# Performance work log

Measured on AMD Instinct MI355X. Metric: run time of the kernel, lower is better.

The kernel has to match this reference:

```python
import jax, jax.numpy as jnp
import numpy as np

N, IN, H, HN = 20000, 256, 128, 4
S, K, B, M = 5, 2, 1024, 16
D = H * HN
ALPHA = 0.2
K_OF_S = np.array([0, 0, 1, 1, 1])  # metapath index for each global step
SPLITS = [(0, 2), (2, 5)]           # step ranges: [0,1,0]->2 steps, [0,2,1,0]->3 steps


def lrelu(z):
    return jnp.where(z >= 0, z, ALPHA * z)


def semantic_attention(z, p1w, p1b, p2w):
    # z: [B, P, D] -> Linear(D,H) -> tanh -> Linear(H,1,no bias) -> softmax over P -> weighted sum
    w = jnp.tanh(jnp.einsum('bpd,hd->bph', z, p1w) + p1b)
    s = jnp.einsum('bph,h->bp', w, p2w)
    beta = jax.nn.softmax(s, axis=1)
    return jnp.einsum('bp,bpd->bd', beta, z)


def setup_inputs():
    key = jax.random.key(0)
    ks = jax.random.split(key, 24)
    def g(k, shape, scale=1.0):
        return jax.random.normal(k, shape, dtype=jnp.float32) * scale
    s_in, s_h, s_d = IN ** -0.5, H ** -0.5, D ** -0.5
    return {
        'x': g(ks[0], (N, IN)),
        'target_nodes_mask': jax.random.randint(ks[1], (B,), 0, N),
        'neighbors': jax.random.randint(ks[2], (S, B, M), 0, N),
        # TransformerLayer params, stacked over (global step, head)
        'fc_w': g(ks[3], (S, HN, H, IN), s_in), 'fc_b': g(ks[4], (S, HN, H), 0.01),
        'q_w': g(ks[5], (S, HN, H, H), s_h), 'q_b': g(ks[6], (S, HN, H), 0.01),
        'k_w': g(ks[7], (S, HN, H, H), s_h), 'k_b': g(ks[8], (S, HN, H), 0.01),
        'v_w': g(ks[9], (S, HN, H, H), s_h), 'v_b': g(ks[10], (S, HN, H), 0.01),
        # AttentionLayer params, stacked over (metapath, head); shared across steps of a metapath
        'att_W': g(ks[11], (K, HN, H, H), s_h),
        'att_fc1_w': g(ks[12], (K, HN, H, H), s_h), 'att_fc1_b': g(ks[13], (K, HN, H), 0.01),
        'att_fc2_w': g(ks[14], (K, HN, H, H), s_h), 'att_fc2_b': g(ks[15], (K, HN, H), 0.01),
        # SemanticAttention params
        'inner_p1_w': g(ks[16], (K, H, D), s_d), 'inner_p1_b': g(ks[17], (K, H), 0.01),
        'inner_p2_w': g(ks[18], (K, H), s_h),
        'btw_p1_w': g(ks[19], (H, D), s_d), 'btw_p1_b': g(ks[20], (H,), 0.01),
        'btw_p2_w': g(ks[21], (H,), s_h),
    }


def reference(x, target_nodes_mask, neighbors, fc_w, fc_b, q_w, q_b, k_w, k_b, v_w, v_b,
              att_W, att_fc1_w, att_fc1_b, att_fc2_w, att_fc2_b,
              inner_p1_w, inner_p1_b, inner_p2_w, btw_p1_w, btw_p1_b, btw_p2_w):
    # eval mode: dropout is identity
    tx = x[target_nodes_mask]                                                             # [B,IN]
    ny = x[neighbors]                                                                     # [S,B,M,IN]
    # shared fc per (step, head) applied to both target and neighbors, then leakyrelu
    x_sh = lrelu(jnp.einsum('bi,shoi->shbo', tx, fc_w) + fc_b[:, :, None, :])             # [S,HN,B,H]
    y_sh = lrelu(jnp.einsum('sbmi,shoi->shbmo', ny, fc_w) + fc_b[:, :, None, None, :])    # [S,HN,B,M,H]
    qh = jnp.einsum('shbd,shod->shbo', x_sh, q_w) + q_b[:, :, None, :]                    # [S,HN,B,H]
    kh = jnp.einsum('shbmd,shod->shbmo', y_sh, k_w) + k_b[:, :, None, None, :]            # [S,HN,B,M,H]
    vh = jnp.einsum('shbmd,shod->shbmo', y_sh, v_w) + v_b[:, :, None, None, :]            # [S,HN,B,M,H]
    # gather per-metapath attention params to per-step layout
    aW, a1w, a1b, a2w, a2b = (p[K_OF_S] for p in (att_W, att_fc1_w, att_fc1_b, att_fc2_w, att_fc2_b))
    # AttentionLayer(key, query): bilinear score h1 @ (W @ h2^T)
    h1 = lrelu(jnp.einsum('shbmd,shod->shbmo', kh, a1w) + a1b[:, :, None, None, :])       # [S,HN,B,M,H]
    h2 = lrelu(jnp.einsum('shbd,shod->shbo', qh, a2w) + a2b[:, :, None, :])               # [S,HN,B,H]
    wh2 = jnp.einsum('shij,shbj->shbi', aW, h2)
    att = jnp.einsum('shbmd,shbd->shbm', h1, wh2)                                         # [S,HN,B,M]
    e = jax.nn.softmax(att, axis=-1)                                                      # softmax over neighbors
    h = jnp.sum(lrelu(vh * e[..., None]), axis=3)                                         # [S,HN,B,H]
    out = (x_sh + h) * 0.5
    out = jnp.transpose(out, (0, 2, 1, 3)).reshape(S, B, D)                               # head concat -> [S,B,D]
    mp = []
    for ki, (s0, s1) in enumerate(SPLITS):
        z = jnp.transpose(out[s0:s1], (1, 0, 2))                                          # [B,P_k,D]
        mp.append(semantic_attention(z, inner_p1_w[ki], inner_p1_b[ki], inner_p2_w[ki]))
    z = jnp.stack(mp, axis=1)                                                             # [B,K,D]
    return semantic_attention(z, btw_p1_w, btw_p1_b, btw_p2_w)                            # [B,D]
```

## Files before the change

kernel.cpp:

```cpp
#include <hip/hip_runtime.h>
#include <hip/hip_bf16.h>

constexpr int IN_ = 256, H_ = 128, HN_ = 4;
constexpr int S_ = 5, B_ = 1024, M_ = 16, D_ = 512;

typedef __attribute__((ext_vector_type(8))) short bf16x8;
typedef __attribute__((ext_vector_type(4))) float f32x4;
typedef __attribute__((ext_vector_type(4))) short s16x4;

__device__ __forceinline__ float lrelu(float z) { return z >= 0.f ? z : 0.2f * z; }
__device__ __forceinline__ short f2b(float f) {
    unsigned u = __float_as_uint(f);
    u += 0x7FFF + ((u >> 16) & 1);
    return (short)(u >> 16);
}
__device__ __forceinline__ float b2f(short s) {
    return __uint_as_float(((unsigned)(unsigned short)s) << 16);
}


template<int K, int ACT, bool TLDS, bool TGLB>
__device__ __forceinline__ void gemm_ldsA(
    const short* A, const short* __restrict__ W, const float* __restrict__ bias,
    short* C_lds, short* __restrict__ C_glob, int lane)
{
    f32x4 acc[8];
#pragma unroll
    for (int i = 0; i < 8; ++i) acc[i] = (f32x4){0.f, 0.f, 0.f, 0.f};
    const int m16 = lane & 15;
    const int kg  = (lane >> 4) * 8;
    const short* Ab = A + m16 * K;
    const int aswz = (m16 & 7) << 3;
#pragma unroll
    for (int kk = 0; kk < K; kk += 32) {
        bf16x8 afr = *(const bf16x8*)(Ab + ((kk + kg) ^ aswz));
        const short* Wb = W + (size_t)m16 * K + kk + kg;
#pragma unroll
        for (int cb = 0; cb < 8; ++cb) {
            bf16x8 bf = *(const bf16x8*)(Wb + (size_t)cb * 16 * K);
            acc[cb] = __builtin_amdgcn_mfma_f32_16x16x32_bf16(afr, bf, acc[cb], 0, 0, 0);
        }
    }
    const int r0 = (lane >> 4) * 4;
#pragma unroll
    for (int cb = 0; cb < 8; ++cb) {
        const int col = cb * 16 + m16;
        const float bv = bias ? bias[col] : 0.f;
#pragma unroll
        for (int i = 0; i < 4; ++i) {
            const int r = r0 + i;
            float v = acc[cb][i] + bv;
            if (ACT) v = lrelu(v);
            const short bs = f2b(v);
            if (TLDS) C_lds[r * H_ + (col ^ ((r & 7) << 3))] = bs;
            if (TGLB) C_glob[(size_t)r * H_ + col] = bs;
        }
    }
}

template<int ACT>
__device__ __forceinline__ void tile_gemm256(
    const short* Asrc, const short* __restrict__ W, const float* __restrict__ bias,
    short* Cdst, int lane, int rbase, int colb)
{
    f32x4 acc[2][2];
#pragma unroll
    for (int a = 0; a < 2; ++a)
#pragma unroll
        for (int b = 0; b < 2; ++b) acc[a][b] = (f32x4){0.f, 0.f, 0.f, 0.f};
    const int m16 = lane & 15, kg = (lane >> 4) * 8;
#pragma unroll
    for (int kk = 0; kk < 8; ++kk) {
        const int k0 = kk * 32 + kg;
        bf16x8 af[2];
#pragma unroll
        for (int rg = 0; rg < 2; ++rg) {
            const int row = rbase + rg * 16 + m16;
            af[rg] = *(const bf16x8*)(Asrc + row * 256 + (k0 ^ ((row & 7) << 3)));
        }
#pragma unroll
        for (int cbl = 0; cbl < 2; ++cbl) {
            const int col = colb + cbl * 16 + m16;
            bf16x8 bf = *(const bf16x8*)(W + (size_t)col * 256 + k0);
#pragma unroll
            for (int rg = 0; rg < 2; ++rg)
                acc[rg][cbl] = __builtin_amdgcn_mfma_f32_16x16x32_bf16(af[rg], bf, acc[rg][cbl], 0, 0, 0);
        }
    }
#pragma unroll
    for (int cbl = 0; cbl < 2; ++cbl) {
        const int col = colb + cbl * 16 + m16;
        const float bv = bias[col];
#pragma unroll
        for (int rg = 0; rg < 2; ++rg)
#pragma unroll
            for (int i = 0; i < 4; ++i) {
                const int row = rbase + rg * 16 + (lane >> 4) * 4 + i;
                float v = acc[rg][cbl][i] + bv;
                if (ACT) v = lrelu(v);
                Cdst[row * 128 + (col ^ ((row & 7) << 3))] = f2b(v);
            }
    }
}

template<int ACT, bool MIDBAR>
__device__ __forceinline__ void tile_gemm128(
    const short* Asrc, const short* __restrict__ W, const float* __restrict__ bias,
    short* Cdst, int lane, int rbase, int colb)
{
    f32x4 acc[2][2];
#pragma unroll
    for (int a = 0; a < 2; ++a)
#pragma unroll
        for (int b = 0; b < 2; ++b) acc[a][b] = (f32x4){0.f, 0.f, 0.f, 0.f};
    const int m16 = lane & 15, kg = (lane >> 4) * 8;
#pragma unroll
    for (int kk = 0; kk < 4; ++kk) {
        const int k0 = kk * 32 + kg;
        bf16x8 af[2];
#pragma unroll
        for (int rg = 0; rg < 2; ++rg) {
            const int row = rbase + rg * 16 + m16;
            af[rg] = *(const bf16x8*)(Asrc + row * 128 + (k0 ^ ((row & 7) << 3)));
        }
#pragma unroll
        for (int cbl = 0; cbl < 2; ++cbl) {
            const int col = colb + cbl * 16 + m16;
            bf16x8 bf = *(const bf16x8*)(W + (size_t)col * 128 + k0);
#pragma unroll
            for (int rg = 0; rg < 2; ++rg)
                acc[rg][cbl] = __builtin_amdgcn_mfma_f32_16x16x32_bf16(af[rg], bf, acc[rg][cbl], 0, 0, 0);
        }
    }
    if (MIDBAR) __syncthreads();
#pragma unroll
    for (int cbl = 0; cbl < 2; ++cbl) {
        const int col = colb + cbl * 16 + m16;
        const float bv = bias[col];
#pragma unroll
        for (int rg = 0; rg < 2; ++rg)
#pragma unroll
            for (int i = 0; i < 4; ++i) {
                const int row = rbase + rg * 16 + (lane >> 4) * 4 + i;
                float v = acc[rg][cbl][i] + bv;
                if (ACT) v = lrelu(v);
                Cdst[row * 128 + (col ^ ((row & 7) << 3))] = f2b(v);
            }
    }
}

__global__ __launch_bounds__(256) void k_convert(
    const float* f0, const float* f1, const float* f2, const float* f3,
    const float* f4, const float* f5, const float* f6,
    short* g0, short* g1, short* g2, short* g3, short* g4, short* g5, short* g6)
{
    const float* s; short* d; int n;
    switch (blockIdx.y) {
        case 0: s = f0; d = g0; n = 655360; break;
        case 1: s = f1; d = g1; n = 327680; break;
        case 2: s = f2; d = g2; n = 327680; break;
        case 3: s = f3; d = g3; n = 327680; break;
        case 4: s = f4; d = g4; n = 131072; break;
        case 5: s = f5; d = g5; n = 131072; break;
        default: s = f6; d = g6; n = 131072; break;
    }
    int i = (blockIdx.x * 256 + threadIdx.x) * 4;
    if (i >= n) return;
    float4 v = *(const float4*)(s + i);
    s16x4 p; p.x = f2b(v.x); p.y = f2b(v.y); p.z = f2b(v.z); p.w = f2b(v.w);
    *(s16x4*)(d + i) = p;
}

__global__ __launch_bounds__(256) void k_transpose(
    const float* __restrict__ ip1w, const float* __restrict__ bp1w,
    float* __restrict__ ipT, float* __restrict__ bpT)
{
    int i = blockIdx.x * 256 + threadIdx.x;
    if (i < 131072) {
        const int d = i & 511, hk = i >> 9;
        const int ki = hk >> 7, h = hk & 127;
        ipT[ki * 65536 + d * 128 + h] = ip1w[i];
    } else if (i < 131072 + 65536) {
        const int j = i - 131072;
        const int d = j & 511, h = j >> 9;
        bpT[d * 128 + h] = bp1w[j];
    }
}

__global__ __launch_bounds__(256) void k_target(
    const float* __restrict__ x, const int* __restrict__ tgt,
    const short* __restrict__ wb_fc, const float* __restrict__ fc_b,
    const short* __restrict__ wb_q,  const float* __restrict__ q_b,
    const short* __restrict__ wb_a2, const float* __restrict__ a2_b,
    const short* __restrict__ wb_aW,
    short* __restrict__ x_shb, short* __restrict__ wh2b)
{
    const int t = threadIdx.x, lane = t & 63, w = t >> 6;
    const int bt = blockIdx.x, s = blockIdx.y;
    const int km = (s < 2) ? 0 : 1;
    const int b0 = bt * 16;
    const int sh = s * HN_ + w, kh = km * HN_ + w;

    __shared__ __align__(16) short A[16 * 256];
    __shared__ __align__(16) short BUF[4 * 2048];
    short* buf0 = BUF + w * 2048;

    {
        const int row = t >> 4, q4 = t & 15;
        const int g = tgt[b0 + row];
        const float* xr = x + (size_t)g * IN_ + q4 * 16;
        short* arow = A + row * 256;
        const int key = (row & 7) << 3;
#pragma unroll
        for (int j = 0; j < 4; ++j) {
            float4 u = *(const float4*)(xr + j * 4);
            const int c = q4 * 16 + j * 4;
            s16x4 p; p.x = f2b(u.x); p.y = f2b(u.y); p.z = f2b(u.z); p.w = f2b(u.w);
            *(s16x4*)(arow + (c ^ key)) = p;
        }
    }
    __syncthreads();

    gemm_ldsA<256, 1, true, true>(A, wb_fc + (size_t)sh * 32768, fc_b + sh * H_,
                                  buf0, x_shb + ((size_t)sh * B_ + b0) * H_, lane);
    gemm_ldsA<128, 0, true, false>(buf0, wb_q + (size_t)sh * 16384, q_b + sh * H_,
                                   buf0, nullptr, lane);
    gemm_ldsA<128, 1, true, false>(buf0, wb_a2 + (size_t)kh * 16384, a2_b + kh * H_,
                                   buf0, nullptr, lane);
    gemm_ldsA<128, 0, false, true>(buf0, wb_aW + (size_t)kh * 16384, nullptr,
                                   nullptr, wh2b + ((size_t)sh * B_ + b0) * H_, lane);
}

__global__ __launch_bounds__(512) void k_fused(
    const float* __restrict__ x, const int* __restrict__ nbr,
    const short* __restrict__ wb_fc, const float* __restrict__ fc_b,
    const short* __restrict__ wb_k,  const float* __restrict__ k_b,
    const short* __restrict__ wb_v,  const float* __restrict__ v_b,
    const short* __restrict__ wb_a1, const float* __restrict__ a1_b,
    const short* __restrict__ x_shb, const short* __restrict__ wh2b,
    float* __restrict__ out_sbd)
{
    const int t = threadIdx.x, lane = t & 63, w = t >> 6;
    const int bt = blockIdx.x, s = blockIdx.y;
    const int km = (s < 2) ? 0 : 1;
    const int r0 = bt * 64;
    const int b0 = bt * 4;
    const int wr = w >> 2;
    const int wc = w & 3;

    __shared__ __align__(16) short A[64 * 256];
    __shared__ __align__(16) short Yt[64 * 128];
    __shared__ __align__(16) short KH[64 * 128];
    __shared__ __align__(16) short VH[64 * 128];

    {
        const int row = t >> 3, q = t & 7;
        const int g = nbr[(size_t)s * (B_ * M_) + r0 + row];
        const float* xr = x + (size_t)g * IN_ + q * 32;
        short* arow = A + row * 256;
        const int key = (row & 7) << 3;
#pragma unroll
        for (int j = 0; j < 8; ++j) {
            float4 u = *(const float4*)(xr + j * 4);
            const int c = q * 32 + j * 4;
            s16x4 p; p.x = f2b(u.x); p.y = f2b(u.y); p.z = f2b(u.z); p.w = f2b(u.w);
            *(s16x4*)(arow + (c ^ key)) = p;
        }
    }
    __syncthreads();

    const int rbase = wr * 32, colb = wc * 32;

    for (int h = 0; h < HN_; ++h) {
        const int sh = s * HN_ + h, kh = km * HN_ + h;

        tile_gemm256<1>(A, wb_fc + (size_t)sh * 32768, fc_b + sh * H_, Yt, lane, rbase, colb);
        __syncthreads();
        tile_gemm128<0, false>(Yt, wb_k + (size_t)sh * 16384, k_b + sh * H_, KH, lane, rbase, colb);
        tile_gemm128<0, false>(Yt, wb_v + (size_t)sh * 16384, v_b + sh * H_, VH, lane, rbase, colb);
        __syncthreads();
        tile_gemm128<1, true>(KH, wb_a1 + (size_t)kh * 16384, a1_b + kh * H_, KH, lane, rbase, colb);
        __syncthreads();

        {
            const int b_loc = w & 3, dhalf = w >> 2;
            const int b = b0 + b_loc;
            const short* wrow = wh2b + ((size_t)sh * B_ + b) * H_;
            const int mloc = lane >> 2;
            const int row  = b_loc * 16 + mloc;
            const int key  = (mloc & 7) << 3;
            float sc = 0.f;
#pragma unroll
            for (int j8 = 0; j8 < 4; ++j8) {
                const int c = (lane & 3) * 32 + j8 * 8;
                bf16x8 hv = *(const bf16x8*)(KH + row * 128 + (c ^ key));
                bf16x8 wv = *(const bf16x8*)(wrow + c);
#pragma unroll
                for (int e2 = 0; e2 < 8; ++e2) sc += b2f(hv[e2]) * b2f(wv[e2]);
            }
            sc += __shfl_xor(sc, 1);
            sc += __shfl_xor(sc, 2);
            float mx = sc;
            mx = fmaxf(mx, __shfl_xor(mx, 4));
            mx = fmaxf(mx, __shfl_xor(mx, 8));
            mx = fmaxf(mx, __shfl_xor(mx, 16));
            mx = fmaxf(mx, __shfl_xor(mx, 32));
            const float es = expf(sc - mx);
            float ss = es;
            ss += __shfl_xor(ss, 4);
            ss += __shfl_xor(ss, 8);
            ss += __shfl_xor(ss, 16);
            ss += __shfl_xor(ss, 32);
            const float inv = 1.f / ss;

            const short* xrow = x_shb + ((size_t)sh * B_ + b) * H_;
            float* orow = out_sbd + ((size_t)s * B_ + b) * D_ + h * H_;
            const int d = dhalf * 64 + lane;
            float hacc = 0.f;
#pragma unroll
            for (int mm = 0; mm < 16; ++mm) {
                const float e_mm = __shfl(es, mm * 4) * inv;
                const float vv = b2f(VH[(b_loc * 16 + mm) * 128 + (d ^ ((mm & 7) << 3))]);
                hacc += lrelu(vv * e_mm);
            }
            orow[d] = (b2f(xrow[d]) + hacc) * 0.5f;
        }
        __syncthreads();
    }
}

__global__ __launch_bounds__(256) void k_semantic(
    const float* __restrict__ out_sbd,
    const float* __restrict__ ipT, const float* __restrict__ ip1b,
    const float* __restrict__ ip2w,
    const float* __restrict__ bpT, const float* __restrict__ bp1b,
    const float* __restrict__ bp2w,
    float* __restrict__ out)
{
    const int b = blockIdx.x, t = threadIdx.x;
    const int h = t & 127, dh = t >> 7;
    __shared__ float zs[S_ * D_];
    __shared__ float red[2 * 128 * 8];
    __shared__ float mps[2 * D_];
    __shared__ float svals[8];
    __shared__ float beta_s[8];

    for (int idx = t; idx < S_ * D_ / 4; idx += 256) {
        int sidx = idx >> 7, c = idx & 127;
        ((float4*)zs)[idx] = ((const float4*)(out_sbd + ((size_t)sidx * B_ + b) * D_))[c];
    }
    __syncthreads();

    {
        float a0 = 0.f, a1 = 0.f, a2 = 0.f, a3 = 0.f, a4 = 0.f;
        const float* w0 = ipT + h;
        const float* w1 = ipT + 65536 + h;
        const int dbeg = dh * 256;
        for (int d = dbeg; d < dbeg + 256; ++d) {
            const float wv0 = w0[d * 128];
            const float wv1 = w1[d * 128];
            a0 += wv0 * zs[d];
            a1 += wv0 * zs[512 + d];
            a2 += wv1 * zs[1024 + d];
            a3 += wv1 * zs[1536 + d];
            a4 += wv1 * zs[2048 + d];
        }
        float* rr = red + (dh * 128 + h) * 8;
        rr[0] = a0; rr[1] = a1; rr[2] = a2; rr[3] = a3; rr[4] = a4;
    }
    __syncthreads();
    if (t < 128) {
#pragma unroll
        for (int p = 0; p < 5; ++p) {
            const int ki = (p < 2) ? 0 : 1;
            float tot = red[t * 8 + p] + red[(128 + t) * 8 + p] + ip1b[ki * 128 + t];
            red[t * 8 + p] = tanhf(tot) * ip2w[ki * 128 + t];
        }
    }
    __syncthreads();
    if (t < 64) {
#pragma unroll
        for (int p = 0; p < 5; ++p) {
            float v = red[t * 8 + p] + red[(t + 64) * 8 + p];
            v += __shfl_xor(v, 1);  v += __shfl_xor(v, 2);  v += __shfl_xor(v, 4);
            v += __shfl_xor(v, 8);  v += __shfl_xor(v, 16); v += __shfl_xor(v, 32);
            if (t == 0) svals[p] = v;
        }
    }
    __syncthreads();
    if (t == 0) {
        float mx = fmaxf(svals[0], svals[1]);
        float e0 = expf(svals[0] - mx), e1 = expf(svals[1] - mx);
        float iv = 1.f / (e0 + e1);
        beta_s[0] = e0 * iv; beta_s[1] = e1 * iv;
        mx = fmaxf(fmaxf(svals[2], svals[3]), svals[4]);
        e0 = expf(svals[2] - mx); e1 = expf(svals[3] - mx); float e2 = expf(svals[4] - mx);
        iv = 1.f / (e0 + e1 + e2);
        beta_s[2] = e0 * iv; beta_s[3] = e1 * iv; beta_s[4] = e2 * iv;
    }
    __syncthreads();
    for (int d = t; d < D_; d += 256) {
        mps[d]       = beta_s[0] * zs[d]        + beta_s[1] * zs[512 + d];
        mps[512 + d] = beta_s[2] * zs[1024 + d] + beta_s[3] * zs[1536 + d] + beta_s[4] * zs[2048 + d];
    }
    __syncthreads();

    {
        float c0 = 0.f, c1 = 0.f;
        const float* wb = bpT + h;
        const int dbeg = dh * 256;
        for (int d = dbeg; d < dbeg + 256; ++d) {
            const float wv = wb[d * 128];
            c0 += wv * mps[d];
            c1 += wv * mps[512 + d];
        }
        float* rr = red + (dh * 128 + h) * 8;
        rr[0] = c0; rr[1] = c1;
    }
    __syncthreads();
    if (t < 128) {
#pragma unroll
        for (int p = 0; p < 2; ++p) {
            float tot = red[t * 8 + p] + red[(128 + t) * 8 + p] + bp1b[t];
            red[t * 8 + p] = tanhf(tot) * bp2w[t];
        }
    }
    __syncthreads();
    if (t < 64) {
#pragma unroll
        for (int p = 0; p < 2; ++p) {
            float v = red[t * 8 + p] + red[(t + 64) * 8 + p];
            v += __shfl_xor(v, 1);  v += __shfl_xor(v, 2);  v += __shfl_xor(v, 4);
            v += __shfl_xor(v, 8);  v += __shfl_xor(v, 16); v += __shfl_xor(v, 32);
            if (t == 0) svals[p] = v;
        }
    }
    __syncthreads();
    if (t == 0) {
        float mx = fmaxf(svals[0], svals[1]);
        float e0 = expf(svals[0] - mx), e1 = expf(svals[1] - mx);
        float iv = 1.f / (e0 + e1);
        beta_s[0] = e0 * iv; beta_s[1] = e1 * iv;
    }
    __syncthreads();
    for (int d = t; d < D_; d += 256)
        out[(size_t)b * D_ + d] = beta_s[0] * mps[d] + beta_s[1] * mps[512 + d];
}

extern "C" void kernel_launch(void* const* d_in, const int* in_sizes, int n_in,
                              void* d_out, int out_size, void* d_ws, size_t ws_size,
                              hipStream_t stream)
{
    const float* x    = (const float*)d_in[0];
    const int*   tgt  = (const int*)d_in[1];
    const int*   nbr  = (const int*)d_in[2];
    const float* fc_w = (const float*)d_in[3];
    const float* fc_b = (const float*)d_in[4];
    const float* q_w  = (const float*)d_in[5];
    const float* q_b  = (const float*)d_in[6];
    const float* k_w  = (const float*)d_in[7];
    const float* k_b  = (const float*)d_in[8];
    const float* v_w  = (const float*)d_in[9];
    const float* v_b  = (const float*)d_in[10];
    const float* attW = (const float*)d_in[11];
    const float* a1w  = (const float*)d_in[12];
    const float* a1b  = (const float*)d_in[13];
    const float* a2w  = (const float*)d_in[14];
    const float* a2b  = (const float*)d_in[15];
    const float* ip1w = (const float*)d_in[16];
    const float* ip1b = (const float*)d_in[17];
    const float* ip2w = (const float*)d_in[18];
    const float* bp1w = (const float*)d_in[19];
    const float* bp1b = (const float*)d_in[20];
    const float* bp2w = (const float*)d_in[21];

    float* out = (float*)d_out;

    short* wb_fc = (short*)d_ws;
    short* wb_q  = wb_fc + 655360;
    short* wb_k  = wb_q + 327680;
    short* wb_v  = wb_k + 327680;
    short* wb_aW = wb_v + 327680;
    short* wb_a1 = wb_aW + 131072;
    short* wb_a2 = wb_a1 + 131072;
    short* x_shb = wb_a2 + 131072;
    short* wh2b  = x_shb + 2621440;
    float* out_sbd = (float*)(wh2b + 2621440);
    float* ipT   = out_sbd + 2621440;
    float* bpT   = ipT + 131072;

    k_convert<<<dim3(640, 7), 256, 0, stream>>>(
        fc_w, q_w, k_w, v_w, attW, a1w, a2w,
        wb_fc, wb_q, wb_k, wb_v, wb_aW, wb_a1, wb_a2);
    k_transpose<<<dim3(768), 256, 0, stream>>>(ip1w, bp1w, ipT, bpT);
    k_target<<<dim3(64, 5), 256, 0, stream>>>(
        x, tgt, wb_fc, fc_b, wb_q, q_b, wb_a2, a2b, wb_aW, x_shb, wh2b);
    k_fused<<<dim3(256, 5), 512, 0, stream>>>(
        x, nbr, wb_fc, fc_b, wb_k, k_b, wb_v, v_b, wb_a1, a1b, x_shb, wh2b, out_sbd);
    k_semantic<<<dim3(B_), 256, 0, stream>>>(
        out_sbd, ipT, ip1b, ip2w, bpT, bp1b, bp2w, out);
}
```

Before: 457.5 us.

## Pre-convert x to bf16 and gather neighbor rows directly from global in fc GEMM

Adds a kernel that converts all of x to bf16 once. The fused kernel then drops its 32KB LDS staging buffer and reads the gathered neighbor rows straight from global memory inside the fc GEMM, which frees LDS for higher occupancy. The a1 output now goes to Yt instead of overwriting KH in place, so the mid-GEMM barrier can be removed. In exchange, the full 20000x256 x is converted every call (about 20MB of fp32 read) even though only gathered rows are needed, and A operands are re-read from global or L2 once per head.

```diff
diff --git a/kernel.cpp b/kernel.cpp
--- a/kernel.cpp
+++ b/kernel.cpp
@@ -59,8 +59,9 @@
 }
 
 template<int ACT>
-__device__ __forceinline__ void tile_gemm256(
-    const short* Asrc, const short* __restrict__ W, const float* __restrict__ bias,
+__device__ __forceinline__ void tile_gemm256g(
+    const short* __restrict__ xr0, const short* __restrict__ xr1,
+    const short* __restrict__ W, const float* __restrict__ bias,
     short* Cdst, int lane, int rbase, int colb)
 {
     f32x4 acc[2][2];
@@ -72,19 +73,14 @@
 #pragma unroll
     for (int kk = 0; kk < 8; ++kk) {
         const int k0 = kk * 32 + kg;
-        bf16x8 af[2];
-#pragma unroll
-        for (int rg = 0; rg < 2; ++rg) {
-            const int row = rbase + rg * 16 + m16;
-            af[rg] = *(const bf16x8*)(Asrc + row * 256 + (k0 ^ ((row & 7) << 3)));
-        }
+        bf16x8 af0 = *(const bf16x8*)(xr0 + kk * 32);
+        bf16x8 af1 = *(const bf16x8*)(xr1 + kk * 32);
 #pragma unroll
         for (int cbl = 0; cbl < 2; ++cbl) {
             const int col = colb + cbl * 16 + m16;
             bf16x8 bf = *(const bf16x8*)(W + (size_t)col * 256 + k0);
-#pragma unroll
-            for (int rg = 0; rg < 2; ++rg)
-                acc[rg][cbl] = __builtin_amdgcn_mfma_f32_16x16x32_bf16(af[rg], bf, acc[rg][cbl], 0, 0, 0);
+            acc[0][cbl] = __builtin_amdgcn_mfma_f32_16x16x32_bf16(af0, bf, acc[0][cbl], 0, 0, 0);
+            acc[1][cbl] = __builtin_amdgcn_mfma_f32_16x16x32_bf16(af1, bf, acc[1][cbl], 0, 0, 0);
         }
     }
 #pragma unroll
@@ -103,7 +99,7 @@
     }
 }
 
-template<int ACT, bool MIDBAR>
+template<int ACT>
 __device__ __forceinline__ void tile_gemm128(
     const short* Asrc, const short* __restrict__ W, const float* __restrict__ bias,
     short* Cdst, int lane, int rbase, int colb)
@@ -132,7 +128,6 @@
                 acc[rg][cbl] = __builtin_amdgcn_mfma_f32_16x16x32_bf16(af[rg], bf, acc[rg][cbl], 0, 0, 0);
         }
     }
-    if (MIDBAR) __syncthreads();
 #pragma unroll
     for (int cbl = 0; cbl < 2; ++cbl) {
         const int col = colb + cbl * 16 + m16;
@@ -171,6 +166,16 @@
     *(s16x4*)(d + i) = p;
 }
 
+__global__ __launch_bounds__(256) void k_convert_x(
+    const float* __restrict__ x, short* __restrict__ xb)
+{
+    int i = (blockIdx.x * 256 + threadIdx.x) * 4;
+    if (i >= 5120000) return;
+    float4 v = *(const float4*)(x + i);
+    s16x4 p; p.x = f2b(v.x); p.y = f2b(v.y); p.z = f2b(v.z); p.w = f2b(v.w);
+    *(s16x4*)(xb + i) = p;
+}
+
 __global__ __launch_bounds__(256) void k_transpose(
     const float* __restrict__ ip1w, const float* __restrict__ bp1w,
     float* __restrict__ ipT, float* __restrict__ bpT)
@@ -232,7 +237,7 @@
 }
 
 __global__ __launch_bounds__(512) void k_fused(
-    const float* __restrict__ x, const int* __restrict__ nbr,
+    const short* __restrict__ xb, const int* __restrict__ nbr,
     const short* __restrict__ wb_fc, const float* __restrict__ fc_b,
     const short* __restrict__ wb_k,  const float* __restrict__ k_b,
     const short* __restrict__ wb_v,  const float* __restrict__ v_b,
@@ -248,38 +253,29 @@
     const int wr = w >> 2;
     const int wc = w & 3;
 
-    __shared__ __align__(16) short A[64 * 256];
     __shared__ __align__(16) short Yt[64 * 128];
     __shared__ __align__(16) short KH[64 * 128];
     __shared__ __align__(16) short VH[64 * 128];
-
-    {
-        const int row = t >> 3, q = t & 7;
-        const int g = nbr[(size_t)s * (B_ * M_) + r0 + row];
-        const float* xr = x + (size_t)g * IN_ + q * 32;
-        short* arow = A + row * 256;
-        const int key = (row & 7) << 3;
-#pragma unroll
-        for (int j = 0; j < 8; ++j) {
-            float4 u = *(const float4*)(xr + j * 4);
-            const int c = q * 32 + j * 4;
-            s16x4 p; p.x = f2b(u.x); p.y = f2b(u.y); p.z = f2b(u.z); p.w = f2b(u.w);
-            *(s16x4*)(arow + (c ^ key)) = p;
-        }
-    }
+    __shared__ int nid[64];
+
+    if (t < 64) nid[t] = nbr[(size_t)s * (B_ * M_) + r0 + t];
     __syncthreads();
 
     const int rbase = wr * 32, colb = wc * 32;
+    const int m16 = lane & 15, kg = (lane >> 4) * 8;
+    const short* xr0 = xb + (size_t)nid[rbase + m16] * 256 + kg;
+    const short* xr1 = xb + (size_t)nid[rbase + 16 + m16] * 256 + kg;
 
     for (int h = 0; h < HN_; ++h) {
         const int sh = s * HN_ + h, kh = km * HN_ + h;
 
-        tile_gemm256<1>(A, wb_fc + (size_t)sh * 32768, fc_b + sh * H_, Yt, lane, rbase, colb);
+        tile_gemm256g<1>(xr0, xr1, wb_fc + (size_t)sh * 32768, fc_b + sh * H_,
+                         Yt, lane, rbase, colb);
         __syncthreads();
-        tile_gemm128<0, false>(Yt, wb_k + (size_t)sh * 16384, k_b + sh * H_, KH, lane, rbase, colb);
-        tile_gemm128<0, false>(Yt, wb_v + (size_t)sh * 16384, v_b + sh * H_, VH, lane, rbase, colb);
+        tile_gemm128<0>(Yt, wb_k + (size_t)sh * 16384, k_b + sh * H_, KH, lane, rbase, colb);
+        tile_gemm128<0>(Yt, wb_v + (size_t)sh * 16384, v_b + sh * H_, VH, lane, rbase, colb);
         __syncthreads();
-        tile_gemm128<1, true>(KH, wb_a1 + (size_t)kh * 16384, a1_b + kh * H_, KH, lane, rbase, colb);
+        tile_gemm128<1>(KH, wb_a1 + (size_t)kh * 16384, a1_b + kh * H_, Yt, lane, rbase, colb);
         __syncthreads();
 
         {
@@ -293,7 +289,7 @@
 #pragma unroll
             for (int j8 = 0; j8 < 4; ++j8) {
                 const int c = (lane & 3) * 32 + j8 * 8;
-                bf16x8 hv = *(const bf16x8*)(KH + row * 128 + (c ^ key));
+                bf16x8 hv = *(const bf16x8*)(Yt + row * 128 + (c ^ key));
                 bf16x8 wv = *(const bf16x8*)(wrow + c);
 #pragma unroll
                 for (int e2 = 0; e2 < 8; ++e2) sc += b2f(hv[e2]) * b2f(wv[e2]);
@@ -488,15 +484,17 @@
     float* out_sbd = (float*)(wh2b + 2621440);
     float* ipT   = out_sbd + 2621440;
     float* bpT   = ipT + 131072;
+    short* xb    = (short*)(bpT + 65536);
 
     k_convert<<<dim3(640, 7), 256, 0, stream>>>(
         fc_w, q_w, k_w, v_w, attW, a1w, a2w,
         wb_fc, wb_q, wb_k, wb_v, wb_aW, wb_a1, wb_a2);
+    k_convert_x<<<dim3(5000), 256, 0, stream>>>(x, xb);
     k_transpose<<<dim3(768), 256, 0, stream>>>(ip1w, bp1w, ipT, bpT);
     k_target<<<dim3(64, 5), 256, 0, stream>>>(
         x, tgt, wb_fc, fc_b, wb_q, q_b, wb_a2, a2b, wb_aW, x_shb, wh2b);
     k_fused<<<dim3(256, 5), 512, 0, stream>>>(
-        x, nbr, wb_fc, fc_b, wb_k, k_b, wb_v, v_b, wb_a1, a1b, x_shb, wh2b, out_sbd);
+        xb, nbr, wb_fc, fc_b, wb_k, k_b, wb_v, v_b, wb_a1, a1b, x_shb, wh2b, out_sbd);
     k_semantic<<<dim3(B_), 256, 0, stream>>>(
         out_sbd, ipT, ip1b, ip2w, bpT, bp1b, bp2w, out);
 }
```

Measured after the change: 486.6 us. +6.4%, slower.

## Precompose key/query projections with attention fc weights into single fused matrices

Applied to the files above, without the earlier changes.

Multiplies a1_w by k_w and a2_w by q_w (and folds the biases) in a new per-call prep kernel. This removes one 128x128 GEMM and one barrier per head from the neighbor kernel, and one GEMM from the target kernel. The k_fused kernel no longer needs the KH LDS buffer, which lowers LDS use and may raise occupancy. In exchange it adds a small fp32 weight-composition kernel on 40 blocks with a 64-float accumulator per thread, and it changes rounding because the composed weights are rounded to bf16 once.

```diff
diff --git a/kernel.cpp b/kernel.cpp
--- a/kernel.cpp
+++ b/kernel.cpp
@@ -150,25 +150,71 @@
 }
 
 __global__ __launch_bounds__(256) void k_convert(
-    const float* f0, const float* f1, const float* f2, const float* f3,
-    const float* f4, const float* f5, const float* f6,
-    short* g0, short* g1, short* g2, short* g3, short* g4, short* g5, short* g6)
+    const float* f0, const float* f1, const float* f2,
+    short* g0, short* g1, short* g2)
 {
     const float* s; short* d; int n;
     switch (blockIdx.y) {
         case 0: s = f0; d = g0; n = 655360; break;
         case 1: s = f1; d = g1; n = 327680; break;
-        case 2: s = f2; d = g2; n = 327680; break;
-        case 3: s = f3; d = g3; n = 327680; break;
-        case 4: s = f4; d = g4; n = 131072; break;
-        case 5: s = f5; d = g5; n = 131072; break;
-        default: s = f6; d = g6; n = 131072; break;
+        default: s = f2; d = g2; n = 131072; break;
     }
     int i = (blockIdx.x * 256 + threadIdx.x) * 4;
     if (i >= n) return;
     float4 v = *(const float4*)(s + i);
     s16x4 p; p.x = f2b(v.x); p.y = f2b(v.y); p.z = f2b(v.z); p.w = f2b(v.w);
     *(s16x4*)(d + i) = p;
+}
+
+__global__ __launch_bounds__(256) void k_fuse_w(
+    const float* __restrict__ a1w, const float* __restrict__ k_w,
+    const float* __restrict__ a1b, const float* __restrict__ k_b,
+    const float* __restrict__ a2w, const float* __restrict__ q_w,
+    const float* __restrict__ a2b, const float* __restrict__ q_b,
+    short* __restrict__ wb_ka, float* __restrict__ ka_b,
+    short* __restrict__ wb_qa, float* __restrict__ qa_b)
+{
+    const int sh = blockIdx.x;
+    const int s = sh >> 2, h = sh & 3;
+    const int kh = ((s < 2) ? 0 : 1) * 4 + h;
+    const float *A, *Bm, *bA, *bB; short* oW; float* oB;
+    if (blockIdx.y == 0) {
+        A = a1w + (size_t)kh * 16384; Bm = k_w + (size_t)sh * 16384;
+        bA = a1b + kh * 128; bB = k_b + sh * 128;
+        oW = wb_ka + (size_t)sh * 16384; oB = ka_b + sh * 128;
+    } else {
+        A = a2w + (size_t)kh * 16384; Bm = q_w + (size_t)sh * 16384;
+        bA = a2b + kh * 128; bB = q_b + sh * 128;
+        oW = wb_qa + (size_t)sh * 16384; oB = qa_b + sh * 128;
+    }
+    __shared__ float Alt[129 * 128];
+    __shared__ float Bl[128 * 128];
+    const int t = threadIdx.x;
+    for (int idx = t; idx < 16384; idx += 256) {
+        const int o = idx >> 7, j = idx & 127;
+        Alt[j * 129 + o] = A[idx];
+    }
+    for (int i = t; i < 4096; i += 256)
+        ((float4*)Bl)[i] = ((const float4*)Bm)[i];
+    __syncthreads();
+
+    const int o = t & 127, half = t >> 7;
+    float acc[64];
+#pragma unroll
+    for (int i = 0; i < 64; ++i) acc[i] = 0.f;
+    for (int j = 0; j < 128; ++j) {
+        const float a = Alt[j * 129 + o];
+        const float* brow = Bl + j * 128 + half * 64;
+#pragma unroll
+        for (int i = 0; i < 64; ++i) acc[i] += a * brow[i];
+    }
+#pragma unroll
+    for (int i = 0; i < 64; ++i) oW[o * 128 + half * 64 + i] = f2b(acc[i]);
+    if (half == 0) {
+        float sb = bA[o];
+        for (int j = 0; j < 128; ++j) sb += Alt[j * 129 + o] * bB[j];
+        oB[o] = sb;
+    }
 }
 
 __global__ __launch_bounds__(256) void k_transpose(
@@ -190,8 +236,7 @@
 __global__ __launch_bounds__(256) void k_target(
     const float* __restrict__ x, const int* __restrict__ tgt,
     const short* __restrict__ wb_fc, const float* __restrict__ fc_b,
-    const short* __restrict__ wb_q,  const float* __restrict__ q_b,
-    const short* __restrict__ wb_a2, const float* __restrict__ a2_b,
+    const short* __restrict__ wb_qa, const float* __restrict__ qa_b,
     const short* __restrict__ wb_aW,
     short* __restrict__ x_shb, short* __restrict__ wh2b)
 {
@@ -223,9 +268,7 @@
 
     gemm_ldsA<256, 1, true, true>(A, wb_fc + (size_t)sh * 32768, fc_b + sh * H_,
                                   buf0, x_shb + ((size_t)sh * B_ + b0) * H_, lane);
-    gemm_ldsA<128, 0, true, false>(buf0, wb_q + (size_t)sh * 16384, q_b + sh * H_,
-                                   buf0, nullptr, lane);
-    gemm_ldsA<128, 1, true, false>(buf0, wb_a2 + (size_t)kh * 16384, a2_b + kh * H_,
+    gemm_ldsA<128, 1, true, false>(buf0, wb_qa + (size_t)sh * 16384, qa_b + sh * H_,
                                    buf0, nullptr, lane);
     gemm_ldsA<128, 0, false, true>(buf0, wb_aW + (size_t)kh * 16384, nullptr,
                                    nullptr, wh2b + ((size_t)sh * B_ + b0) * H_, lane);
@@ -234,23 +277,19 @@
 __global__ __launch_bounds__(512) void k_fused(
     const float* __restrict__ x, const int* __restrict__ nbr,
     const short* __restrict__ wb_fc, const float* __restrict__ fc_b,
-    const short* __restrict__ wb_k,  const float* __restrict__ k_b,
     const short* __restrict__ wb_v,  const float* __restrict__ v_b,
-    const short* __restrict__ wb_a1, const float* __restrict__ a1_b,
+    const short* __restrict__ wb_ka, const float* __restrict__ ka_b,
     const short* __restrict__ x_shb, const short* __restrict__ wh2b,
     float* __restrict__ out_sbd)
 {
     const int t = threadIdx.x, lane = t & 63, w = t >> 6;
     const int bt = blockIdx.x, s = blockIdx.y;
-    const int km = (s < 2) ? 0 : 1;
     const int r0 = bt * 64;
     const int b0 = bt * 4;
-    const int wr = w >> 2;
-    const int wc = w & 3;
+    const int wr = w >> 2, wc = w & 3;
 
     __shared__ __align__(16) short A[64 * 256];
     __shared__ __align__(16) short Yt[64 * 128];
-    __shared__ __align__(16) short KH[64 * 128];
     __shared__ __align__(16) short VH[64 * 128];
 
     {
@@ -272,14 +311,12 @@
     const int rbase = wr * 32, colb = wc * 32;
 
     for (int h = 0; h < HN_; ++h) {
-        const int sh = s * HN_ + h, kh = km * HN_ + h;
+        const int sh = s * HN_ + h;
 
         tile_gemm256<1>(A, wb_fc + (size_t)sh * 32768, fc_b + sh * H_, Yt, lane, rbase, colb);
         __syncthreads();
-        tile_gemm128<0, false>(Yt, wb_k + (size_t)sh * 16384, k_b + sh * H_, KH, lane, rbase, colb);
         tile_gemm128<0, false>(Yt, wb_v + (size_t)sh * 16384, v_b + sh * H_, VH, lane, rbase, colb);
-        __syncthreads();
-        tile_gemm128<1, true>(KH, wb_a1 + (size_t)kh * 16384, a1_b + kh * H_, KH, lane, rbase, colb);
+        tile_gemm128<1, true>(Yt, wb_ka + (size_t)sh * 16384, ka_b + sh * H_, Yt, lane, rbase, colb);
         __syncthreads();
 
         {
@@ -293,7 +330,7 @@
 #pragma unroll
             for (int j8 = 0; j8 < 4; ++j8) {
                 const int c = (lane & 3) * 32 + j8 * 8;
-                bf16x8 hv = *(const bf16x8*)(KH + row * 128 + (c ^ key));
+                bf16x8 hv = *(const bf16x8*)(Yt + row * 128 + (c ^ key));
                 bf16x8 wv = *(const bf16x8*)(wrow + c);
 #pragma unroll
                 for (int e2 = 0; e2 < 8; ++e2) sc += b2f(hv[e2]) * b2f(wv[e2]);
@@ -477,26 +514,27 @@
     float* out = (float*)d_out;
 
     short* wb_fc = (short*)d_ws;
-    short* wb_q  = wb_fc + 655360;
-    short* wb_k  = wb_q + 327680;
-    short* wb_v  = wb_k + 327680;
+    short* wb_v  = wb_fc + 655360;
     short* wb_aW = wb_v + 327680;
-    short* wb_a1 = wb_aW + 131072;
-    short* wb_a2 = wb_a1 + 131072;
-    short* x_shb = wb_a2 + 131072;
+    short* wb_ka = wb_aW + 131072;
+    short* wb_qa = wb_ka + 327680;
+    short* x_shb = wb_qa + 327680;
     short* wh2b  = x_shb + 2621440;
-    float* out_sbd = (float*)(wh2b + 2621440);
+    float* ka_b  = (float*)(wh2b + 2621440);
+    float* qa_b  = ka_b + 2560;
+    float* out_sbd = qa_b + 2560;
     float* ipT   = out_sbd + 2621440;
     float* bpT   = ipT + 131072;
 
-    k_convert<<<dim3(640, 7), 256, 0, stream>>>(
-        fc_w, q_w, k_w, v_w, attW, a1w, a2w,
-        wb_fc, wb_q, wb_k, wb_v, wb_aW, wb_a1, wb_a2);
+    k_convert<<<dim3(640, 3), 256, 0, stream>>>(
+        fc_w, v_w, attW, wb_fc, wb_v, wb_aW);
+    k_fuse_w<<<dim3(20, 2), 256, 0, stream>>>(
+        a1w, k_w, a1b, k_b, a2w, q_w, a2b, q_b, wb_ka, ka_b, wb_qa, qa_b);
     k_transpose<<<dim3(768), 256, 0, stream>>>(ip1w, bp1w, ipT, bpT);
     k_target<<<dim3(64, 5), 256, 0, stream>>>(
-        x, tgt, wb_fc, fc_b, wb_q, q_b, wb_a2, a2b, wb_aW, x_shb, wh2b);
+        x, tgt, wb_fc, fc_b, wb_qa, qa_b, wb_aW, x_shb, wh2b);
     k_fused<<<dim3(256, 5), 512, 0, stream>>>(
-        x, nbr, wb_fc, fc_b, wb_k, k_b, wb_v, v_b, wb_a1, a1b, x_shb, wh2b, out_sbd);
+        x, nbr, wb_fc, fc_b, wb_v, v_b, wb_ka, ka_b, x_shb, wh2b, out_sbd);
     k_semantic<<<dim3(B_), 256, 0, stream>>>(
         out_sbd, ipT, ip1b, ip2w, bpT, bp1b, bp2w, out);
 }
```

New measurement: 436.4 us. 4.6% less time.
